# Optimization experiments

Measured on AMD Instinct MI355X. Metric: run time of the kernel, lower is better.

The kernel has to match this reference:

```python
import jax, jax.numpy as jnp
import numpy as np
import math

H, KV, D = 32, 8, 128  # n_head, num_key_value_heads, head_dim
ROPE_BASE = 10000.0

def rotate_half(x):
    x1, x2 = x[..., : x.shape[-1] // 2], x[..., x.shape[-1] // 2 :]
    return jnp.concatenate((-x2, x1), axis=-1)

def setup_inputs() -> dict:
    key = jax.random.key(0)
    ks = jax.random.split(key, 5)
    B, T, C = 2, 2048, 4096
    x = jax.random.normal(ks[0], (B, T, C), dtype=jnp.float32)
    # causal additive mask: 1 where masked (strictly upper triangular)
    mask = jnp.triu(jnp.ones((T, T), dtype=jnp.float32), k=1)
    s = 0.02
    wq = jax.random.normal(ks[1], (C, H * D), dtype=jnp.float32) * s
    wk = jax.random.normal(ks[2], (C, KV * D), dtype=jnp.float32) * s
    wv = jax.random.normal(ks[3], (C, KV * D), dtype=jnp.float32) * s
    wo = jax.random.normal(ks[4], (C, C), dtype=jnp.float32) * s
    return {"x": x, "mask": mask, "wq": wq, "wk": wk, "wv": wv, "wo": wo}

def reference(x, mask, wq, wk, wv, wo):
    B, T, C = x.shape
    n_rep = H // KV
    q = jnp.einsum('btc,ch->bth', x, wq).reshape(B, T, H, D).transpose(0, 2, 1, 3)
    k = jnp.einsum('btc,ch->bth', x, wk).reshape(B, T, KV, D).transpose(0, 2, 1, 3)
    v = jnp.einsum('btc,ch->bth', x, wv).reshape(B, T, KV, D).transpose(0, 2, 1, 3)
    # RoPE; faithful to source: freqs = sum over batch of inv_freq*pos = B * inv_freq * t
    inv_freq = 1.0 / (ROPE_BASE ** (jnp.arange(0, D, 2, dtype=jnp.float32) / D))
    freqs = (jnp.arange(T, dtype=jnp.float32)[:, None] * inv_freq[None, :]) * B  # [T, D/2]
    emb = jnp.concatenate((freqs, freqs), axis=-1)  # [T, D]
    cos, sin = jnp.cos(emb).astype(x.dtype), jnp.sin(emb).astype(x.dtype)
    q = q * cos + rotate_half(q) * sin
    k = k * cos + rotate_half(k) * sin
    # GQA repeat_kv
    k = jnp.repeat(k, n_rep, axis=1)
    v = jnp.repeat(v, n_rep, axis=1)
    scores = jnp.einsum('bhtd,bhsd->bhts', q, k) / math.sqrt(D)
    scores = scores + mask * (-1e9)
    attn = jax.nn.softmax(scores, axis=-1)
    y = jnp.einsum('bhts,bhsd->bhtd', attn, v)
    y = y.transpose(0, 2, 1, 3).reshape(B, T, C)
    return jnp.einsum('btc,co->bto', y, wo)
```

## Files before the change

### kernel.cpp

```cpp
#include <hip/hip_runtime.h>
#include <cstdint>
#include <cstddef>

typedef float  f32x4  __attribute__((ext_vector_type(4)));
typedef __bf16 bf16x8 __attribute__((ext_vector_type(8)));
typedef __bf16 bf16x4 __attribute__((ext_vector_type(4)));

#define AS1CV(p) ((const __attribute__((address_space(1))) void*)(uintptr_t)(p))
#define AS3V(p)  ((__attribute__((address_space(3))) void*)(uintptr_t)(p))
#define LGKM0()  asm volatile("s_waitcnt lgkmcnt(0)" ::: "memory")

__global__ __launch_bounds__(256) void convert_k(
    const float* __restrict__ in, __bf16* __restrict__ out, long n)
{
  const long i = ((long)blockIdx.x * 256 + threadIdx.x) * 4;
  if (i + 3 < n) {
    float4 v = *(const float4*)(in + i);
    __bf16 e[4] = { (__bf16)v.x, (__bf16)v.y, (__bf16)v.z, (__bf16)v.w };
    *(uint2*)(out + i) = *(const uint2*)e;
  }
}

__global__ __launch_bounds__(256) void transpose_f32_bf16_k(
    const float* __restrict__ in, __bf16* __restrict__ out, long inRow, long outRow)
{
  const long tr = (long)blockIdx.y * 64;
  const long tc = (long)blockIdx.x * 64;
  __shared__ float tile[64][65];
  const int tid = threadIdx.x;
  const int rr = tid >> 4, c4 = (tid & 15) * 4;
#pragma unroll
  for (int p = 0; p < 4; p++) {
    const int r = p * 16 + rr;
    float4 v = *(const float4*)(in + (tr + r) * inRow + tc + c4);
    tile[r][c4]     = v.x;
    tile[r][c4 + 1] = v.y;
    tile[r][c4 + 2] = v.z;
    tile[r][c4 + 3] = v.w;
  }
  __syncthreads();
#pragma unroll
  for (int p = 0; p < 2; p++) {
    const int u  = p * 256 + tid;
    const int oc = u >> 3, ch = (u & 7) * 8;
    unsigned short e[8];
#pragma unroll
    for (int j = 0; j < 8; j++) {
      __bf16 b = (__bf16)tile[ch + j][oc];
      e[j] = *(unsigned short*)&b;
    }
    *(uint4*)(out + (tc + oc) * outRow + tr + ch) = *(const uint4*)e;
  }
}

__global__ __launch_bounds__(256) void transpose_bf16_k(
    const __bf16* __restrict__ in, __bf16* __restrict__ out,
    long inRow, long outRow,
    int sliceDiv, long sliceOuter, long sliceInner, long outSlice)
{
  const int s = blockIdx.z;
  const __bf16* ip = in + (long)(s / sliceDiv) * sliceOuter + (long)(s % sliceDiv) * sliceInner;
  __bf16* op = out + (long)s * outSlice;
  const long tr = (long)blockIdx.y * 64;
  const long tc = (long)blockIdx.x * 64;
  __shared__ unsigned short tile[64][66];
  const int tid = threadIdx.x;
  const int rr  = tid >> 3;
  const int c8  = (tid & 7) * 8;
#pragma unroll
  for (int p = 0; p < 2; p++) {
    const int r = p * 32 + rr;
    uint4 v = *(const uint4*)(ip + (tr + r) * inRow + tc + c8);
    const unsigned short* e = (const unsigned short*)&v;
#pragma unroll
    for (int j = 0; j < 8; j++) tile[r][c8 + j] = e[j];
  }
  __syncthreads();
#pragma unroll
  for (int p = 0; p < 2; p++) {
    const int c = p * 32 + rr;
    unsigned short e[8];
#pragma unroll
    for (int j = 0; j < 8; j++) e[j] = tile[c8 + j][c];
    *(uint4*)(op + (tc + c) * outRow + tr + c8) = *(const uint4*)e;
  }
}

template <typename OutT, int NR>
__global__ __launch_bounds__(512, 2) void gemm256(
    const __bf16* __restrict__ A, const __bf16* __restrict__ BT,
    OutT* __restrict__ C, int M, int N, int K)
{
  constexpr int BN   = NR * 64;
  constexpr int NB   = NR;
  constexpr int ABUF = 256 * 64;
  constexpr int BBUF = BN * 64;
  const int n0   = blockIdx.x * BN;
  const int m0   = blockIdx.y * 256;
  const int tid  = threadIdx.x;
  const int lane = tid & 63;
  const int wave = tid >> 6;
  const int quad = lane >> 4;
  const int r    = lane & 15;
  const int wm   = wave >> 2;
  const int wn   = wave & 3;

  __shared__ __bf16 a_sm[2 * ABUF];
  __shared__ __bf16 b_sm[2 * BBUF];

  f32x4 acc[8][NR] = {};

  const int srow = tid >> 3;
  const int schk = ((tid & 7) ^ (srow & 7)) * 8;
  const __bf16* aSrc = A  + (size_t)(m0 + srow) * K + schk;
  const __bf16* bSrc = BT + (size_t)(n0 + srow) * K + schk;
  const size_t rstep = (size_t)64 * K;
  const int wofs = wave * 512;
  const int NT = K >> 6;

  auto stageA = [&](int si, int ko, int dstbuf) {
    __builtin_amdgcn_global_load_lds(AS1CV(aSrc + si * rstep + ko),
                                     AS3V(a_sm + dstbuf + si * 4096 + wofs), 16, 0, 0);
  };
  auto stageB = [&](int si, int ko, int dstbuf) {
    __builtin_amdgcn_global_load_lds(AS1CV(bSrc + si * rstep + ko),
                                     AS3V(b_sm + dstbuf + si * 4096 + wofs), 16, 0, 0);
  };

#pragma unroll
  for (int si = 0; si < NB; si++) stageB(si, 0, 0);
  stageA(0, 0, 0); stageA(2, 0, 0); stageA(1, 0, 0); stageA(3, 0, 0);
  asm volatile("s_waitcnt vmcnt(2)" ::: "memory");
  __builtin_amdgcn_sched_barrier(0);
  __builtin_amdgcn_s_barrier();

#pragma unroll 2
  for (int t = 0; t < NT; ++t) {
    const int abuf = (t & 1) ? ABUF : 0;
    const int bbuf = (t & 1) ? BBUF : 0;
    const int anb  = abuf ^ ABUF;
    const int bnb  = bbuf ^ BBUF;
    const int kn   = ((t + 1 < NT) ? (t + 1) : t) * 64;
    const __bf16* as = a_sm + abuf + (wm * 128 + r) * 64;
    const __bf16* bs = b_sm + bbuf + (wn * (NR * 16) + r) * 64;
    bf16x8 bfr[NR][2];

#pragma unroll
    for (int p = 0; p < 4; p++) {
      if (p == 0) {
#pragma unroll
        for (int ni = 0; ni < NR; ni++)
#pragma unroll
          for (int kk = 0; kk < 2; kk++)
            bfr[ni][kk] = *(const bf16x8*)(bs + ni * 1024 + (((kk * 4 + quad) ^ (r & 7)) * 8));
      }
      bf16x8 af[2][2];
#pragma unroll
      for (int u = 0; u < 2; u++)
#pragma unroll
        for (int kk = 0; kk < 2; kk++)
          af[u][kk] = *(const bf16x8*)(as + (p * 2 + u) * 1024 + (((kk * 4 + quad) ^ (r & 7)) * 8));

      if (p == 0) { stageB(0, kn, bnb); stageB(1, kn, bnb); }
      if (p == 1) {
        if constexpr (NR == 3) { stageB(2, kn, bnb); stageA(0, kn, anb); }
        else                   { stageB(2, kn, bnb); stageB(3, kn, bnb); }
      }
      if (p == 2) {
        if constexpr (NR == 3) { stageA(2, kn, anb); stageA(1, kn, anb); }
        else                   { stageA(0, kn, anb); stageA(2, kn, anb); }
      }
      if (p == 3) {
        if constexpr (NR == 3) { stageA(3, kn, anb); }
        else                   { stageA(1, kn, anb); stageA(3, kn, anb); }
      }

      __builtin_amdgcn_s_barrier();
      __builtin_amdgcn_s_setprio(1);
#pragma unroll
      for (int u = 0; u < 2; u++)
#pragma unroll
        for (int ni = 0; ni < NR; ni++)
#pragma unroll
          for (int kk = 0; kk < 2; kk++)
            acc[p * 2 + u][ni] = __builtin_amdgcn_mfma_f32_16x16x32_bf16(af[u][kk], bfr[ni][kk], acc[p * 2 + u][ni], 0, 0, 0);
      __builtin_amdgcn_s_setprio(0);
      if (p == 1) { asm volatile("s_waitcnt vmcnt(4)" ::: "memory"); __builtin_amdgcn_sched_barrier(0); }
      if (p == 3) { asm volatile("s_waitcnt vmcnt(2)" ::: "memory"); __builtin_amdgcn_sched_barrier(0); }
      __builtin_amdgcn_s_barrier();
    }
  }
  asm volatile("s_waitcnt vmcnt(0)" ::: "memory");

#pragma unroll
  for (int mi = 0; mi < 8; mi++)
#pragma unroll
    for (int ni = 0; ni < NR; ni++) {
      const int col = n0 + wn * (NR * 16) + ni * 16 + r;
#pragma unroll
      for (int g = 0; g < 4; g++) {
        const int row = m0 + wm * 128 + mi * 16 + quad * 4 + g;
        C[(size_t)row * N + col] = (OutT)acc[mi][ni][g];
      }
    }
}

__global__ __launch_bounds__(256) void rope_k(
    const __bf16* __restrict__ qkv, __bf16* __restrict__ qr, __bf16* __restrict__ kr)
{
  const int m = blockIdx.x;
  const int b = m >> 11;
  const int t = m & 2047;
  const __bf16* rowp = qkv + (size_t)m * 6144;
  for (int n = threadIdx.x; n < 5120; n += 256) {
    const bool isq  = n < 4096;
    const int local = isq ? n : (n - 4096);
    const int head  = local >> 7;
    const int d     = local & 127;
    const int j     = d & 63;
    const float ex   = (float)(2 * j) / 128.0f;
    const float invf = 1.0f / powf(10000.0f, ex);
    const float ang  = ((float)t * invf) * 2.0f;
    const float c = cosf(ang), s = sinf(ang);
    const float v0 = (float)rowp[n];
    const float v1 = (float)rowp[n + ((d < 64) ? 64 : -64)];
    const float o  = (d < 64) ? (v0 * c - v1 * s) : (v0 * c + v1 * s);
    if (isq) qr[((size_t)(b * 32 + head) * 2048 + t) * 128 + d] = (__bf16)o;
    else     kr[((size_t)(b * 8  + head) * 2048 + t) * 128 + d] = (__bf16)o;
  }
}

__global__ __launch_bounds__(256, 3) void flash_k(
    const __bf16* __restrict__ qr, const __bf16* __restrict__ kr,
    const __bf16* __restrict__ vT, __bf16* __restrict__ y)
{
  const int qt  = (int)gridDim.x - 1 - (int)blockIdx.x;
  const int bh  = blockIdx.y;
  const int b   = bh >> 5;
  const int h   = bh & 31;
  const int kvh = h >> 2;
  const int tq0 = qt * 64;
  const int tid  = threadIdx.x;
  const int lane = tid & 63;
  const int wave = tid >> 6;
  const int quad = lane >> 4;
  const int r    = lane & 15;

  __shared__ __bf16 k_sm[64 * 128];
  __shared__ __bf16 v_sm[128 * 64];
  __shared__ __bf16 p_sm[4][16 * 64];
  __shared__ float  al_sm[64];
  __shared__ float  l_sm[64];

  const __bf16* kbase = kr + ((size_t)(b * 8 + kvh) * 2048) * 128;
  const __bf16* vbase = vT + ((size_t)(b * 8 + kvh) * 128) * 2048;

  bf16x8 qf[4];
  {
    const __bf16* qrow = qr + ((size_t)(b * 32 + h) * 2048 + tq0 + wave * 16 + r) * 128;
#pragma unroll
    for (int kk = 0; kk < 4; kk++)
      qf[kk] = *(const bf16x8*)(qrow + kk * 32 + quad * 8);
  }

  f32x4 Oacc[8] = {};
  float mstate = -1e30f, lstate = 0.0f;
  const float scale = 0.08838834764831845f;

  const int rowK = lane >> 4, cK = lane & 15;
  const int rowV = lane >> 3, cV = lane & 7;

  for (int jt = 0; jt <= qt; jt++) {
    __syncthreads();
#pragma unroll
    for (int i = 0; i < 4; i++) {
      const int li = wave * 4 + i;
      {
        const int row = li * 4 + rowK;
        const __bf16* g = kbase + (size_t)(jt * 64 + row) * 128 + ((cK ^ (row & 15)) * 8);
        __builtin_amdgcn_global_load_lds(AS1CV(g), AS3V(k_sm + li * 512), 16, 0, 0);
      }
      {
        const int row = li * 8 + rowV;
        const __bf16* g = vbase + (size_t)row * 2048 + jt * 64 + ((cV ^ (row & 7)) * 8);
        __builtin_amdgcn_global_load_lds(AS1CV(g), AS3V(v_sm + li * 512), 16, 0, 0);
      }
    }
    __syncthreads();

    f32x4 St[4] = {};
#pragma unroll
    for (int kk = 0; kk < 4; kk++)
#pragma unroll
      for (int mi = 0; mi < 4; mi++) {
        bf16x8 kf = *(const bf16x8*)(k_sm + (mi * 16 + r) * 128 + (((kk * 4 + quad) ^ r) * 8));
        St[mi] = __builtin_amdgcn_mfma_f32_16x16x32_bf16(kf, qf[kk], St[mi], 0, 0, 0);
      }

    const bool diag = (jt == qt);
    const int qabs  = tq0 + wave * 16 + r;
    float p[16];
#pragma unroll
    for (int mi = 0; mi < 4; mi++)
#pragma unroll
      for (int g = 0; g < 4; g++) {
        float v = St[mi][g] * scale;
        if (diag && (jt * 64 + mi * 16 + quad * 4 + g) > qabs) v = -3.0e38f;
        p[mi * 4 + g] = v;
      }
    float mx = p[0];
#pragma unroll
    for (int i = 1; i < 16; i++) mx = fmaxf(mx, p[i]);
    mx = fmaxf(mx, __shfl_xor(mx, 16));
    mx = fmaxf(mx, __shfl_xor(mx, 32));
    const float mnew  = fmaxf(mstate, mx);
    const float alpha = __expf(mstate - mnew);
    mstate = mnew;
    float rs = 0.0f;
#pragma unroll
    for (int i = 0; i < 16; i++) { p[i] = __expf(p[i] - mnew); rs += p[i]; }
    rs += __shfl_xor(rs, 16);
    rs += __shfl_xor(rs, 32);
    lstate = lstate * alpha + rs;
    if (quad == 0) al_sm[wave * 16 + r] = alpha;

#pragma unroll
    for (int mi = 0; mi < 4; mi++) {
      bf16x4 pk = { (__bf16)p[mi*4+0], (__bf16)p[mi*4+1], (__bf16)p[mi*4+2], (__bf16)p[mi*4+3] };
      const int cw = mi * 2 + (quad >> 1);
      *(bf16x4*)(&p_sm[wave][r * 64 + ((cw ^ (r & 7)) * 8) + (quad & 1) * 4]) = pk;
    }
    LGKM0();

    {
      const float a0 = al_sm[wave * 16 + quad * 4 + 0];
      const float a1 = al_sm[wave * 16 + quad * 4 + 1];
      const float a2 = al_sm[wave * 16 + quad * 4 + 2];
      const float a3 = al_sm[wave * 16 + quad * 4 + 3];
#pragma unroll
      for (int dt = 0; dt < 8; dt++) {
        Oacc[dt][0] *= a0; Oacc[dt][1] *= a1; Oacc[dt][2] *= a2; Oacc[dt][3] *= a3;
      }
    }

#pragma unroll
    for (int kk = 0; kk < 2; kk++) {
      bf16x8 pf = *(const bf16x8*)(&p_sm[wave][r * 64 + (((kk * 4 + quad) ^ (r & 7)) * 8)]);
#pragma unroll
      for (int dt = 0; dt < 8; dt++) {
        bf16x8 vf = *(const bf16x8*)(v_sm + (dt * 16 + r) * 64 + (((kk * 4 + quad) ^ (r & 7)) * 8));
        Oacc[dt] = __builtin_amdgcn_mfma_f32_16x16x32_bf16(pf, vf, Oacc[dt], 0, 0, 0);
      }
    }
  }

  if (quad == 0) l_sm[wave * 16 + r] = lstate;
  LGKM0();
  const float il0 = 1.0f / l_sm[wave * 16 + quad * 4 + 0];
  const float il1 = 1.0f / l_sm[wave * 16 + quad * 4 + 1];
  const float il2 = 1.0f / l_sm[wave * 16 + quad * 4 + 2];
  const float il3 = 1.0f / l_sm[wave * 16 + quad * 4 + 3];
#pragma unroll
  for (int dt = 0; dt < 8; dt++) {
    const int col = h * 128 + dt * 16 + r;
    const int row = tq0 + wave * 16 + quad * 4;
    y[((size_t)(b * 2048 + row + 0)) * 4096 + col] = (__bf16)(Oacc[dt][0] * il0);
    y[((size_t)(b * 2048 + row + 1)) * 4096 + col] = (__bf16)(Oacc[dt][1] * il1);
    y[((size_t)(b * 2048 + row + 2)) * 4096 + col] = (__bf16)(Oacc[dt][2] * il2);
    y[((size_t)(b * 2048 + row + 3)) * 4096 + col] = (__bf16)(Oacc[dt][3] * il3);
  }
}

extern "C" void kernel_launch(void* const* d_in, const int* in_sizes, int n_in,
                              void* d_out, int out_size, void* d_ws, size_t ws_size,
                              hipStream_t stream)
{
  const float* x  = (const float*)d_in[0];
  const float* wq = (const float*)d_in[2];
  const float* wk = (const float*)d_in[3];
  const float* wv = (const float*)d_in[4];
  const float* wo = (const float*)d_in[5];
  float* out = (float*)d_out;

  __bf16* ws  = (__bf16*)d_ws;
  __bf16* xb  = ws;
  __bf16* wT  = xb  + (size_t)16777216;
  __bf16* qkv = wT  + (size_t)25165824;
  __bf16* qr  = qkv + (size_t)25165824;
  __bf16* kr  = qr  + (size_t)16777216;
  __bf16* vT  = kr  + (size_t)4194304;
  __bf16* y   = xb;
  __bf16* woT = wT;

  dim3 blk(256);
  convert_k<<<dim3(16384), blk, 0, stream>>>(x, xb, 16777216L);
  transpose_f32_bf16_k<<<dim3(64, 64), blk, 0, stream>>>(wq, wT,                     4096L, 4096L);
  transpose_f32_bf16_k<<<dim3(16, 64), blk, 0, stream>>>(wk, wT + (size_t)4096*4096, 1024L, 4096L);
  transpose_f32_bf16_k<<<dim3(16, 64), blk, 0, stream>>>(wv, wT + (size_t)5120*4096, 1024L, 4096L);
  gemm256<__bf16, 3><<<dim3(32, 16), dim3(512), 0, stream>>>(xb, wT, qkv, 4096, 6144, 4096);
  transpose_f32_bf16_k<<<dim3(64, 64), blk, 0, stream>>>(wo, woT, 4096L, 4096L);
  rope_k<<<dim3(4096), blk, 0, stream>>>(qkv, qr, kr);
  transpose_bf16_k<<<dim3(2, 32, 16), blk, 0, stream>>>(qkv + 5120, vT, 6144L, 2048L,
                                                        8, (long)2048 * 6144, 128L, (long)128 * 2048);
  flash_k<<<dim3(32, 64), blk, 0, stream>>>(qr, kr, vT, y);
  gemm256<float, 4><<<dim3(16, 16), dim3(512), 0, stream>>>(y, woT, out, 4096, 4096, 4096);
}
```

Measured before the change: 815.4 us.

## Prefetch next K/V tile into registers during attention compute

Replaces the direct global-to-LDS K/V loads with register prefetch of the next tile, issued before the current tile's QK and PV MFMAs and written to LDS after a barrier. The aim is to hide global load latency behind compute. It also swaps the LDS round trips for alpha and l with wave shuffles and raises wave priority around the MFMA blocks. In exchange it costs extra VGPRs for the staging registers, which may lower occupancy, and adds a second barrier per iteration.

```diff
diff --git a/kernel.cpp b/kernel.cpp
--- a/kernel.cpp
+++ b/kernel.cpp
@@ -249,8 +249,6 @@
   __shared__ __bf16 k_sm[64 * 128];
   __shared__ __bf16 v_sm[128 * 64];
   __shared__ __bf16 p_sm[4][16 * 64];
-  __shared__ float  al_sm[64];
-  __shared__ float  l_sm[64];
 
   const __bf16* kbase = kr + ((size_t)(b * 8 + kvh) * 2048) * 128;
   const __bf16* vbase = vT + ((size_t)(b * 8 + kvh) * 128) * 2048;
@@ -270,25 +268,37 @@
   const int rowK = lane >> 4, cK = lane & 15;
   const int rowV = lane >> 3, cV = lane & 7;
 
-  for (int jt = 0; jt <= qt; jt++) {
-    __syncthreads();
+  uint4 kreg[4], vreg[4];
+  auto loadKV = [&](int jt) {
 #pragma unroll
     for (int i = 0; i < 4; i++) {
       const int li = wave * 4 + i;
-      {
-        const int row = li * 4 + rowK;
-        const __bf16* g = kbase + (size_t)(jt * 64 + row) * 128 + ((cK ^ (row & 15)) * 8);
-        __builtin_amdgcn_global_load_lds(AS1CV(g), AS3V(k_sm + li * 512), 16, 0, 0);
-      }
-      {
-        const int row = li * 8 + rowV;
-        const __bf16* g = vbase + (size_t)row * 2048 + jt * 64 + ((cV ^ (row & 7)) * 8);
-        __builtin_amdgcn_global_load_lds(AS1CV(g), AS3V(v_sm + li * 512), 16, 0, 0);
-      }
-    }
-    __syncthreads();
+      const int rk = li * 4 + rowK;
+      kreg[i] = *(const uint4*)(kbase + (size_t)(jt * 64 + rk) * 128 + ((cK ^ (rk & 15)) * 8));
+      const int rv = li * 8 + rowV;
+      vreg[i] = *(const uint4*)(vbase + (size_t)rv * 2048 + jt * 64 + ((cV ^ (rv & 7)) * 8));
+    }
+  };
+  auto writeKV = [&]() {
+#pragma unroll
+    for (int i = 0; i < 4; i++) {
+      const int li = wave * 4 + i;
+      *(uint4*)(k_sm + li * 512 + lane * 8) = kreg[i];
+      *(uint4*)(v_sm + li * 512 + lane * 8) = vreg[i];
+    }
+  };
+
+  loadKV(0);
+  writeKV();
+  __syncthreads();
+
+  for (int jt = 0; jt <= qt; jt++) {
+    const bool pf = (jt < qt);
+    if (pf) loadKV(jt + 1);
+    __builtin_amdgcn_sched_barrier(0);
 
     f32x4 St[4] = {};
+    __builtin_amdgcn_s_setprio(1);
 #pragma unroll
     for (int kk = 0; kk < 4; kk++)
 #pragma unroll
@@ -296,6 +306,7 @@
         bf16x8 kf = *(const bf16x8*)(k_sm + (mi * 16 + r) * 128 + (((kk * 4 + quad) ^ r) * 8));
         St[mi] = __builtin_amdgcn_mfma_f32_16x16x32_bf16(kf, qf[kk], St[mi], 0, 0, 0);
       }
+    __builtin_amdgcn_s_setprio(0);
 
     const bool diag = (jt == qt);
     const int qabs  = tq0 + wave * 16 + r;
@@ -322,7 +333,6 @@
     rs += __shfl_xor(rs, 16);
     rs += __shfl_xor(rs, 32);
     lstate = lstate * alpha + rs;
-    if (quad == 0) al_sm[wave * 16 + r] = alpha;
 
 #pragma unroll
     for (int mi = 0; mi < 4; mi++) {
@@ -333,33 +343,37 @@
     LGKM0();
 
     {
-      const float a0 = al_sm[wave * 16 + quad * 4 + 0];
-      const float a1 = al_sm[wave * 16 + quad * 4 + 1];
-      const float a2 = al_sm[wave * 16 + quad * 4 + 2];
-      const float a3 = al_sm[wave * 16 + quad * 4 + 3];
+      const float a0 = __shfl(alpha, quad * 4 + 0);
+      const float a1 = __shfl(alpha, quad * 4 + 1);
+      const float a2 = __shfl(alpha, quad * 4 + 2);
+      const float a3 = __shfl(alpha, quad * 4 + 3);
 #pragma unroll
       for (int dt = 0; dt < 8; dt++) {
         Oacc[dt][0] *= a0; Oacc[dt][1] *= a1; Oacc[dt][2] *= a2; Oacc[dt][3] *= a3;
       }
     }
 
+    __builtin_amdgcn_s_setprio(1);
 #pragma unroll
     for (int kk = 0; kk < 2; kk++) {
-      bf16x8 pf = *(const bf16x8*)(&p_sm[wave][r * 64 + (((kk * 4 + quad) ^ (r & 7)) * 8)]);
+      bf16x8 pf_ = *(const bf16x8*)(&p_sm[wave][r * 64 + (((kk * 4 + quad) ^ (r & 7)) * 8)]);
 #pragma unroll
       for (int dt = 0; dt < 8; dt++) {
         bf16x8 vf = *(const bf16x8*)(v_sm + (dt * 16 + r) * 64 + (((kk * 4 + quad) ^ (r & 7)) * 8));
-        Oacc[dt] = __builtin_amdgcn_mfma_f32_16x16x32_bf16(pf, vf, Oacc[dt], 0, 0, 0);
-      }
-    }
-  }
-
-  if (quad == 0) l_sm[wave * 16 + r] = lstate;
-  LGKM0();
-  const float il0 = 1.0f / l_sm[wave * 16 + quad * 4 + 0];
-  const float il1 = 1.0f / l_sm[wave * 16 + quad * 4 + 1];
-  const float il2 = 1.0f / l_sm[wave * 16 + quad * 4 + 2];
-  const float il3 = 1.0f / l_sm[wave * 16 + quad * 4 + 3];
+        Oacc[dt] = __builtin_amdgcn_mfma_f32_16x16x32_bf16(pf_, vf, Oacc[dt], 0, 0, 0);
+      }
+    }
+    __builtin_amdgcn_s_setprio(0);
+
+    __syncthreads();
+    if (pf) writeKV();
+    __syncthreads();
+  }
+
+  const float il0 = 1.0f / __shfl(lstate, quad * 4 + 0);
+  const float il1 = 1.0f / __shfl(lstate, quad * 4 + 1);
+  const float il2 = 1.0f / __shfl(lstate, quad * 4 + 2);
+  const float il3 = 1.0f / __shfl(lstate, quad * 4 + 3);
 #pragma unroll
   for (int dt = 0; dt < 8; dt++) {
     const int col = h * 128 + dt * 16 + r;
```

Result: slower. 1.199 ms (+47.1%).
